# Optimization experiments

Hardware: AMD Instinct MI355X
Metric: run time of the kernel (lower is better)

The kernel has to match this reference:

```python
import jax, jax.numpy as jnp
import numpy as np
from jax import lax

TOP_K = 4
ROUTED_SCALING = 1.0
RENORMALIZE = True


def setup_inputs() -> dict:
    key = jax.random.key(0)
    ks = jax.random.split(key, 9)
    H, I, E = 2048, 1024, 16
    s = 0.02
    return {
        "hidden_states": jax.random.normal(ks[0], (2, 1024, H), jnp.float32),
        "gate_w": jax.random.normal(ks[1], (E, H), jnp.float32) * s,
        "expert_bias": jax.random.normal(ks[2], (E,), jnp.float32) * s,
        "w_gate": jax.random.normal(ks[3], (E, I, H), jnp.float32) * s,
        "w_up": jax.random.normal(ks[4], (E, I, H), jnp.float32) * s,
        "w_down": jax.random.normal(ks[5], (E, H, I), jnp.float32) * s,
        "sw_gate": jax.random.normal(ks[6], (I, H), jnp.float32) * s,
        "sw_up": jax.random.normal(ks[7], (I, H), jnp.float32) * s,
        "sw_down": jax.random.normal(ks[8], (H, I), jnp.float32) * s,
    }


def _swiglu_ffn(x, wg, wu, wd):
    # SiluAndMul(gate_up) -> down_proj
    return (jax.nn.silu(x @ wg.T) * (x @ wu.T)) @ wd.T


def reference(hidden_states, gate_w, expert_bias, w_gate, w_up, w_down,
              sw_gate, sw_up, sw_down):
    orig_shape = hidden_states.shape
    H = orig_shape[-1]
    x = hidden_states.reshape(-1, H)            # [T, H]
    T = x.shape[0]

    # --- sigmoid gating with score-correction bias (bias affects selection only) ---
    logits = x.astype(jnp.float32) @ gate_w.T    # [T, E] fp32 router
    scores = jax.nn.sigmoid(logits)
    _, topk_idx = lax.top_k(scores + expert_bias[None, :], TOP_K)   # [T, K]
    topk_w = jnp.take_along_axis(scores, topk_idx, axis=-1)         # raw scores
    if RENORMALIZE:
        topk_w = topk_w / jnp.sum(topk_w, axis=-1, keepdims=True)
    topk_w = topk_w * ROUTED_SCALING

    # scatter top-k weights into dense [T, E] combine matrix
    E = gate_w.shape[0]
    combine = jnp.zeros((T, E), dtype=x.dtype).at[
        jnp.arange(T)[:, None], topk_idx].set(topk_w.astype(x.dtype))

    # --- routed experts: scan over experts, weighted accumulate ---
    def step(acc, ws):
        wg, wu, wd, cw = ws                     # cw: [T] combine weights
        return acc + cw[:, None] * _swiglu_ffn(x, wg, wu, wd), None

    routed, _ = lax.scan(step, jnp.zeros_like(x),
                         (w_gate, w_up, w_down, combine.T))

    # --- shared expert ---
    shared = _swiglu_ffn(x, sw_gate, sw_up, sw_down)

    return (routed + shared).reshape(orig_shape)
```

## Files before the change

kernel.cpp:

```cpp
#include <hip/hip_runtime.h>
#include <hip/hip_bf16.h>
#include <cstdint>

#define TK 2048
#define HD 2048
#define ID 1024
#define NE 16
#define NG 17
#define TOPK 4
#define SLOTS (TK*TOPK)
#define ROWS_ALL (SLOTS+TK)
#define IH (ID*HD)
#define MAXT 96

typedef __attribute__((ext_vector_type(4))) float f32x4;
typedef __attribute__((ext_vector_type(16))) float f32x16;
typedef __attribute__((ext_vector_type(8))) short s16x8;
typedef unsigned short u16;
typedef unsigned long long u64;

__device__ __forceinline__ u16 f2bf(float f){
  union { float f; uint32_t u; } v; v.f = f;
  uint32_t r = v.u + 0x7fffu + ((v.u >> 16) & 1u);
  return (u16)(r >> 16);
}

#define GLD16(g, l) __builtin_amdgcn_global_load_lds( \
    (const __attribute__((address_space(1))) void*)(g), \
    (__attribute__((address_space(3))) void*)(l), 16, 0, 0)

__device__ __forceinline__ const s16x8* fragp(const u16* b, int row, int off){
  return (const s16x8*)((const char*)b + row*128 + (off ^ ((row&7)<<4)));
}
__device__ __forceinline__ int swz2(int r){
  return (r & 7) ^ (((r >> 3) & 3) << 1);
}
__device__ __forceinline__ const s16x8* fragp2(const u16* b, int row, int off){
  return (const s16x8*)((const char*)b + row*128 + (off ^ (swz2(row)<<4)));
}

#define MFMA16(a,b,c) __builtin_amdgcn_mfma_f32_16x16x32_bf16((a),(b),(c),0,0,0)
#define MFMA32(a,b,c) __builtin_amdgcn_mfma_f32_32x32x16_bf16((a),(b),(c),0,0,0)

__global__ void k_prep(const float* __restrict__ x, u16* __restrict__ xb,
                       u64* __restrict__ maskbits, int* __restrict__ tokcnt){
  int gi = blockIdx.x*blockDim.x + threadIdx.x;
  int st = gridDim.x*blockDim.x;
  if (gi < NE*32) maskbits[gi] = 0ull;
  if (gi < TK) tokcnt[gi] = 0;
  for (int i=gi; i<TK*HD/4; i+=st){
    float4 f = ((const float4*)x)[i];
    ushort4 o; o.x=f2bf(f.x); o.y=f2bf(f.y); o.z=f2bf(f.z); o.w=f2bf(f.w);
    ((ushort4*)xb)[i] = o;
  }
}

__global__ void k_cvtw(const float* __restrict__ wg, const float* __restrict__ wu,
                       const float* __restrict__ wd, const float* __restrict__ swg,
                       const float* __restrict__ swu, const float* __restrict__ swd,
                       u16* __restrict__ wgb, u16* __restrict__ wub, u16* __restrict__ wdb){
  const size_t nbig = (size_t)NE*IH/4, nsml = IH/4;
  const size_t total = 3*nbig + 3*nsml;
  for (size_t i = (size_t)blockIdx.x*blockDim.x + threadIdx.x; i < total;
       i += (size_t)gridDim.x*blockDim.x){
    const float4* src; ushort4* dst; size_t j = i;
    if (j < nbig){ src=(const float4*)wg + j;  dst=(ushort4*)wgb + j; }
    else if ((j-=nbig) < nbig){ src=(const float4*)wu + j;  dst=(ushort4*)wub + j; }
    else if ((j-=nbig) < nbig){ src=(const float4*)wd + j;  dst=(ushort4*)wdb + j; }
    else if ((j-=nbig) < nsml){ src=(const float4*)swg + j; dst=(ushort4*)wgb + nbig + j; }
    else if ((j-=nsml) < nsml){ src=(const float4*)swu + j; dst=(ushort4*)wub + nbig + j; }
    else { j-=nsml; src=(const float4*)swd + j; dst=(ushort4*)wdb + nbig + j; }
    float4 f = *src;
    ushort4 o; o.x=f2bf(f.x); o.y=f2bf(f.y); o.z=f2bf(f.z); o.w=f2bf(f.w);
    *dst = o;
  }
}

__global__ __launch_bounds__(256) void k_logits(const float* __restrict__ x,
                                                const float* __restrict__ gw,
                                                const float* __restrict__ bias,
                                                float* __restrict__ wdense,
                                                u64* __restrict__ maskbits){
  int t = blockIdx.x, tid = threadIdx.x;
  int lane = tid & 63, wv = tid >> 6;
  const float* xr = x + (size_t)t*HD;
  float acc[NE];
  #pragma unroll
  for (int e=0;e<NE;e++) acc[e]=0.f;
  for (int k=tid;k<HD;k+=256){
    float xv = xr[k];
    #pragma unroll
    for (int e=0;e<NE;e++) acc[e] += xv * gw[e*HD + k];
  }
  __shared__ float red[NE][4];
  #pragma unroll
  for (int e=0;e<NE;e++){
    float v = acc[e];
    #pragma unroll
    for (int off=32;off>0;off>>=1) v += __shfl_down(v, off, 64);
    if (lane==0) red[e][wv] = v;
  }
  __syncthreads();
  if (tid == 0){
    float sc[NE], bs[NE];
    #pragma unroll
    for (int e=0;e<NE;e++){
      float l = red[e][0]+red[e][1]+red[e][2]+red[e][3];
      float s = 1.f/(1.f+expf(-l));
      sc[e]=s; bs[e]=s+bias[e];
    }
    int idx[TOPK]; float wsum=0.f; unsigned used=0;
    for (int k=0;k<TOPK;k++){
      int best=0; float bv=-1e30f;
      for (int e=0;e<NE;e++) if (!((used>>e)&1u) && bs[e] > bv){ bv=bs[e]; best=e; }
      used |= 1u<<best; idx[k]=best; wsum += sc[best];
    }
    float inv = 1.f/wsum;
    for (int k=0;k<TOPK;k++){
      int e = idx[k];
      wdense[t*NE + e] = sc[e]*inv;
      atomicOr(&maskbits[e*32 + (t>>6)], 1ull << (t&63));
    }
  }
}

__global__ void k_scan(const u64* __restrict__ maskbits, int* __restrict__ counts,
                       int* __restrict__ offsets, int* __restrict__ wordpfx,
                       int* __restrict__ tiles){
  int acc = 0;
  for (int e=0;e<NE;e++){
    int c = 0;
    for (int w=0;w<32;w++){ wordpfx[e*32+w] = c; c += __popcll(maskbits[e*32+w]); }
    counts[e] = c;
  }
  for (int e=0;e<NE;e++){ offsets[e] = acc; acc += counts[e]; }
  offsets[NE] = acc;
  counts[NE] = TK;
  int nt = 0;
  for (int g=0; g<NG; g++){
    int c = counts[g];
    for (int mt=0; mt*128 < c && nt < MAXT; mt++) tiles[nt++] = (g<<8) | mt;
  }
  for (; nt<MAXT; nt++) tiles[nt] = -1;
}

__global__ void k_scatter(const u64* __restrict__ maskbits, const int* __restrict__ offsets,
                          const int* __restrict__ wordpfx, const float* __restrict__ wdense,
                          int* __restrict__ rowtok, float* __restrict__ roww,
                          int* __restrict__ tokcnt, int* __restrict__ tok4){
  int t = blockIdx.x*blockDim.x + threadIdx.x;
  int e = blockIdx.y;
  if (t >= TK) return;
  if (e == NE){ rowtok[offsets[NE]+t] = t; roww[offsets[NE]+t] = 1.f; return; }
  u64 w = maskbits[e*32 + (t>>6)];
  if ((w >> (t&63)) & 1ull){
    int pos = offsets[e] + wordpfx[e*32 + (t>>6)] + __popcll(w & ((1ull << (t&63)) - 1ull));
    rowtok[pos] = t; roww[pos] = wdense[t*NE + e];
    int r = atomicAdd(&tokcnt[t], 1);
    tok4[t*TOPK + r] = pos;
  }
}

__global__ __launch_bounds__(256) void k_gemm1b(
    const u16* __restrict__ xb, const u16* __restrict__ wgb, const u16* __restrict__ wub,
    const int* __restrict__ counts, const int* __restrict__ offsets,
    const int* __restrict__ rowtok, const float* __restrict__ roww,
    const int* __restrict__ tiles, u16* __restrict__ P)
{
  int te = tiles[blockIdx.y];
  if (te < 0) return;
  int g = te >> 8, mt = te & 255;
  int cnt = counts[g];
  int n0 = blockIdx.x*64;
  int base = offsets[g];
  const u16* wg16 = wgb + (size_t)g*IH;
  const u16* wu16 = wub + (size_t)g*IH;

  __shared__ u16 lsA[128*64];
  __shared__ u16 lsG[64*64];
  __shared__ u16 lsU[64*64];

  int tid = threadIdx.x, lane = tid & 63, wv = tid >> 6;
  int wm = (wv>>1)*64, wn = (wv&1)*32;
  int rl = lane & 15, hi = lane >> 4;

  f32x4 accg[4][2] = {}; f32x4 accu[4][2] = {};

  const u16* aSrc[4];
  #pragma unroll
  for (int i=0;i<4;i++){
    int b = i*256 + tid, r = b>>3, cb = b&7;
    int m = mt*128 + r; if (m >= cnt) m = cnt-1;
    int tok = rowtok[base + m];
    aSrc[i] = xb + (size_t)tok*HD + ((cb ^ (r&7))<<3);
  }
  const u16 *gSrc[2], *uSrc[2];
  #pragma unroll
  for (int i=0;i<2;i++){
    int b = i*256 + tid, r = b>>3, cb = b&7;
    size_t off = (size_t)(n0 + r)*HD + ((cb ^ (r&7))<<3);
    gSrc[i] = wg16 + off; uSrc[i] = wu16 + off;
  }

  for (int k0=0; k0<HD; k0+=64){
    #pragma unroll
    for (int i=0;i<4;i++) GLD16(aSrc[i]+k0, lsA + (i*256 + wv*64)*8);
    #pragma unroll
    for (int i=0;i<2;i++) GLD16(gSrc[i]+k0, lsG + (i*256 + wv*64)*8);
    #pragma unroll
    for (int i=0;i<2;i++) GLD16(uSrc[i]+k0, lsU + (i*256 + wv*64)*8);
    __syncthreads();
    #pragma unroll
    for (int ks=0; ks<2; ++ks){
      int off = ks*64 + hi*16;
      s16x8 af[4];
      #pragma unroll
      for (int mi=0;mi<4;mi++) af[mi] = *fragp(lsA, wm+16*mi+rl, off);
      #pragma unroll
      for (int ni=0;ni<2;ni++){
        s16x8 bg = *fragp(lsG, wn+16*ni+rl, off);
        s16x8 bu = *fragp(lsU, wn+16*ni+rl, off);
        #pragma unroll
        for (int mi=0;mi<4;mi++){
          accg[mi][ni] = MFMA16(af[mi], bg, accg[mi][ni]);
          accu[mi][ni] = MFMA16(af[mi], bu, accu[mi][ni]);
        }
      }
    }
    __syncthreads();
  }
  int rl4 = hi*4, cl = rl;
  #pragma unroll
  for (int mi=0;mi<4;mi++){
    #pragma unroll
    for (int j=0;j<4;j++){
      int m = mt*128 + wm + mi*16 + rl4 + j;
      if (m < cnt){
        int slot = base + m;
        float wgt = roww[slot];
        #pragma unroll
        for (int ni=0;ni<2;ni++){
          float gv = accg[mi][ni][j], uv = accu[mi][ni][j];
          float pv = gv/(1.f+expf(-gv))*uv*wgt;
          P[(size_t)slot*ID + n0 + wn + ni*16 + cl] = f2bf(pv);
        }
      }
    }
  }
}

__global__ __launch_bounds__(256, 2) void k_gemm2b(
    const u16* __restrict__ P, const u16* __restrict__ wdb,
    const int* __restrict__ counts, const int* __restrict__ offsets,
    const int* __restrict__ tiles, u16* __restrict__ R)
{
  int te = tiles[blockIdx.y];
  if (te < 0) return;
  int g = te >> 8, mt = te & 255;
  int cnt = counts[g];
  int base = offsets[g];
  int n0 = blockIdx.x*256;
  const u16* wd16 = wdb + (size_t)g*IH;

  __shared__ u16 lsA[128*64];
  __shared__ u16 lsB[256*64];

  int tid = threadIdx.x, lane = tid & 63, wv = tid >> 6;
  int wm = (wv>>1)*64, wn = (wv&1)*128;
  int rl = lane & 31, hi = lane >> 5;
  f32x16 acc[2][4] = {};

  const u16* aSrc[4];
  #pragma unroll
  for (int i=0;i<4;i++){
    int b = i*256 + tid, r = b>>3, cb = b&7;
    int m = mt*128 + r; if (m >= cnt) m = cnt-1;
    aSrc[i] = P + (size_t)(base + m)*ID + ((cb ^ swz2(r))<<3);
  }
  const u16* bSrc[8];
  #pragma unroll
  for (int i=0;i<8;i++){
    int b = i*256 + tid, r = b>>3, cb = b&7;
    bSrc[i] = wd16 + (size_t)(n0 + r)*ID + ((cb ^ swz2(r))<<3);
  }

  for (int t=0; t<ID/64; ++t){
    int k0 = t*64;
    #pragma unroll
    for (int i=0;i<4;i++) GLD16(aSrc[i]+k0, lsA + (i*256 + wv*64)*8);
    #pragma unroll
    for (int i=0;i<8;i++) GLD16(bSrc[i]+k0, lsB + (i*256 + wv*64)*8);
    asm volatile("s_waitcnt vmcnt(0)" ::: "memory");
    __builtin_amdgcn_s_barrier();
    #pragma unroll
    for (int s=0; s<4; ++s){
      int off = s*32 + hi*16;
      s16x8 af[2], bf[4];
      af[0] = *fragp2(lsA, wm + rl, off);
      af[1] = *fragp2(lsA, wm + 32 + rl, off);
      #pragma unroll
      for (int nj=0;nj<4;nj++) bf[nj] = *fragp2(lsB, wn + nj*32 + rl, off);
      #pragma unroll
      for (int mi=0;mi<2;mi++)
        #pragma unroll
        for (int nj=0;nj<4;nj++)
          acc[mi][nj] = MFMA32(af[mi], bf[nj], acc[mi][nj]);
    }
    asm volatile("s_waitcnt lgkmcnt(0)" ::: "memory");
    __builtin_amdgcn_s_barrier();
  }
  #pragma unroll
  for (int mi=0;mi<2;mi++){
    #pragma unroll
    for (int r=0;r<16;r++){
      int rowb = wm + mi*32 + (r&3) + 8*(r>>2) + 4*hi;
      int m = mt*128 + rowb;
      if (m < cnt){
        int slot = base + m;
        u16* rrow = R + (size_t)slot*HD + n0 + wn + rl;
        #pragma unroll
        for (int nj=0;nj<4;nj++) rrow[nj*32] = f2bf(acc[mi][nj][r]);
      }
    }
  }
}

__global__ __launch_bounds__(256) void k_reduce(const u16* __restrict__ R,
                                                const int* __restrict__ tok4,
                                                float* __restrict__ out){
  int t = blockIdx.x;
  int c0 = threadIdx.x * 8;
  int s0 = tok4[t*TOPK+0], s1 = tok4[t*TOPK+1], s2 = tok4[t*TOPK+2], s3 = tok4[t*TOPK+3];
  const ushort4* p0 = (const ushort4*)(R + (size_t)s0*HD + c0);
  const ushort4* p1 = (const ushort4*)(R + (size_t)s1*HD + c0);
  const ushort4* p2 = (const ushort4*)(R + (size_t)s2*HD + c0);
  const ushort4* p3 = (const ushort4*)(R + (size_t)s3*HD + c0);
  const ushort4* ps = (const ushort4*)(R + (size_t)(SLOTS + t)*HD + c0);
  float* o = out + (size_t)t*HD + c0;
  #pragma unroll
  for (int h=0; h<2; h++){
    ushort4 a = p0[h], b = p1[h], c = p2[h], d = p3[h], e = ps[h];
    #pragma unroll
    for (int j=0;j<4;j++){
      u16 ua = ((const u16*)&a)[j], ub = ((const u16*)&b)[j];
      u16 uc = ((const u16*)&c)[j], ud = ((const u16*)&d)[j], ue = ((const u16*)&e)[j];
      union { uint32_t u; float f; } w;
      float v;
      w.u = (uint32_t)ua<<16; v  = w.f;
      w.u = (uint32_t)ub<<16; v += w.f;
      w.u = (uint32_t)uc<<16; v += w.f;
      w.u = (uint32_t)ud<<16; v += w.f;
      w.u = (uint32_t)ue<<16; v += w.f;
      o[h*4 + j] = v;
    }
  }
}


extern "C" void kernel_launch(void* const* d_in, const int* in_sizes, int n_in,
                              void* d_out, int out_size, void* d_ws, size_t ws_size,
                              hipStream_t stream){
  (void)in_sizes; (void)n_in; (void)ws_size; (void)out_size;
  const float* x       = (const float*)d_in[0];
  const float* gate_w  = (const float*)d_in[1];
  const float* ebias   = (const float*)d_in[2];
  const float* w_gate  = (const float*)d_in[3];
  const float* w_up    = (const float*)d_in[4];
  const float* w_down  = (const float*)d_in[5];
  const float* sw_gate = (const float*)d_in[6];
  const float* sw_up   = (const float*)d_in[7];
  const float* sw_down = (const float*)d_in[8];
  float* out = (float*)d_out;

  char* p = (char*)d_ws;
  auto alloc = [&](size_t bytes)->char*{ char* r = p; p += (bytes + 255) & ~(size_t)255; return r; };
  u16*   xb       = (u16*)  alloc((size_t)TK*HD*2);
  u16*   P        = (u16*)  alloc((size_t)ROWS_ALL*ID*2);
  float* wdense   = (float*)alloc((size_t)TK*NE*4);
  u64*   maskbits = (u64*)  alloc((size_t)NE*32*8);
  int*   wordpfx  = (int*)  alloc((size_t)NE*32*4);
  int*   counts   = (int*)  alloc(64);
  int*   offsets  = (int*)  alloc(64);
  int*   tiles    = (int*)  alloc(MAXT*4);
  int*   rowtok   = (int*)  alloc((size_t)ROWS_ALL*4);
  float* roww     = (float*)alloc((size_t)ROWS_ALL*4);
  int*   tokcnt   = (int*)  alloc((size_t)TK*4);
  int*   tok4     = (int*)  alloc((size_t)TK*TOPK*4);
  size_t slab = (size_t)NG*IH*2;
  u16* wgb = (u16*)alloc(slab);
  u16* wub = (u16*)alloc(slab);
  u16* wdb = (u16*)alloc(slab);
  u16* R = wgb;

  k_prep<<<2048, 256, 0, stream>>>(x, xb, maskbits, tokcnt);
  k_cvtw<<<2048, 256, 0, stream>>>(w_gate, w_up, w_down, sw_gate, sw_up, sw_down,
                                   wgb, wub, wdb);
  k_logits<<<TK, 256, 0, stream>>>(x, gate_w, ebias, wdense, maskbits);
  k_scan<<<1, 1, 0, stream>>>(maskbits, counts, offsets, wordpfx, tiles);
  k_scatter<<<dim3(TK/256, NG), 256, 0, stream>>>(maskbits, offsets, wordpfx, wdense,
                                                  rowtok, roww, tokcnt, tok4);

  dim3 g1(ID/64, MAXT);
  k_gemm1b<<<g1, 256, 0, stream>>>(xb, wgb, wub, counts, offsets, rowtok, roww, tiles, P);
  dim3 g2(HD/256, MAXT);
  k_gemm2b<<<g2, 256, 0, stream>>>(P, wdb, counts, offsets, tiles, R);
  k_reduce<<<TK, 256, 0, stream>>>(R, tok4, out);
}
```

Measured before the change: 393.6 us.

## Fuse router logits with weight/activation conversion and swizzle GEMM tile order

Merges the activation bf16 conversion, the weight conversion and the router logits/top-k kernel into one launch: the first TK blocks do routing while the remaining blocks convert x and all weights. A small init kernel now zeroes the mask bits and counters. Both grouped GEMMs also remap their flat block index so that groups of 8 row tiles sweep the column tiles together, which should improve L2 reuse of weight tiles. This cuts launch count and lets routing overlap the memory-bound conversion, but the routing blocks may compete with the conversion blocks for bandwidth.

```diff
diff --git a/kernel.cpp b/kernel.cpp
--- a/kernel.cpp
+++ b/kernel.cpp
@@ -42,84 +42,82 @@
 #define MFMA16(a,b,c) __builtin_amdgcn_mfma_f32_16x16x32_bf16((a),(b),(c),0,0,0)
 #define MFMA32(a,b,c) __builtin_amdgcn_mfma_f32_32x32x16_bf16((a),(b),(c),0,0,0)
 
-__global__ void k_prep(const float* __restrict__ x, u16* __restrict__ xb,
-                       u64* __restrict__ maskbits, int* __restrict__ tokcnt){
+__global__ void k_init(u64* __restrict__ maskbits, int* __restrict__ tokcnt){
   int gi = blockIdx.x*blockDim.x + threadIdx.x;
-  int st = gridDim.x*blockDim.x;
   if (gi < NE*32) maskbits[gi] = 0ull;
   if (gi < TK) tokcnt[gi] = 0;
-  for (int i=gi; i<TK*HD/4; i+=st){
-    float4 f = ((const float4*)x)[i];
-    ushort4 o; o.x=f2bf(f.x); o.y=f2bf(f.y); o.z=f2bf(f.z); o.w=f2bf(f.w);
-    ((ushort4*)xb)[i] = o;
-  }
-}
-
-__global__ void k_cvtw(const float* __restrict__ wg, const float* __restrict__ wu,
-                       const float* __restrict__ wd, const float* __restrict__ swg,
-                       const float* __restrict__ swu, const float* __restrict__ swd,
-                       u16* __restrict__ wgb, u16* __restrict__ wub, u16* __restrict__ wdb){
-  const size_t nbig = (size_t)NE*IH/4, nsml = IH/4;
-  const size_t total = 3*nbig + 3*nsml;
-  for (size_t i = (size_t)blockIdx.x*blockDim.x + threadIdx.x; i < total;
-       i += (size_t)gridDim.x*blockDim.x){
-    const float4* src; ushort4* dst; size_t j = i;
-    if (j < nbig){ src=(const float4*)wg + j;  dst=(ushort4*)wgb + j; }
-    else if ((j-=nbig) < nbig){ src=(const float4*)wu + j;  dst=(ushort4*)wub + j; }
-    else if ((j-=nbig) < nbig){ src=(const float4*)wd + j;  dst=(ushort4*)wdb + j; }
-    else if ((j-=nbig) < nsml){ src=(const float4*)swg + j; dst=(ushort4*)wgb + nbig + j; }
-    else if ((j-=nsml) < nsml){ src=(const float4*)swu + j; dst=(ushort4*)wub + nbig + j; }
-    else { j-=nsml; src=(const float4*)swd + j; dst=(ushort4*)wdb + nbig + j; }
-    float4 f = *src;
-    ushort4 o; o.x=f2bf(f.x); o.y=f2bf(f.y); o.z=f2bf(f.z); o.w=f2bf(f.w);
-    *dst = o;
-  }
-}
-
-__global__ __launch_bounds__(256) void k_logits(const float* __restrict__ x,
-                                                const float* __restrict__ gw,
-                                                const float* __restrict__ bias,
-                                                float* __restrict__ wdense,
-                                                u64* __restrict__ maskbits){
-  int t = blockIdx.x, tid = threadIdx.x;
-  int lane = tid & 63, wv = tid >> 6;
-  const float* xr = x + (size_t)t*HD;
-  float acc[NE];
-  #pragma unroll
-  for (int e=0;e<NE;e++) acc[e]=0.f;
-  for (int k=tid;k<HD;k+=256){
-    float xv = xr[k];
-    #pragma unroll
-    for (int e=0;e<NE;e++) acc[e] += xv * gw[e*HD + k];
-  }
-  __shared__ float red[NE][4];
-  #pragma unroll
-  for (int e=0;e<NE;e++){
-    float v = acc[e];
-    #pragma unroll
-    for (int off=32;off>0;off>>=1) v += __shfl_down(v, off, 64);
-    if (lane==0) red[e][wv] = v;
-  }
-  __syncthreads();
-  if (tid == 0){
-    float sc[NE], bs[NE];
+}
+
+__global__ __launch_bounds__(256) void k_fused(
+    const float* __restrict__ x, const float* __restrict__ gw,
+    const float* __restrict__ bias,
+    const float* __restrict__ wg, const float* __restrict__ wu,
+    const float* __restrict__ wd, const float* __restrict__ swg,
+    const float* __restrict__ swu, const float* __restrict__ swd,
+    u16* __restrict__ xb, u16* __restrict__ wgb, u16* __restrict__ wub,
+    u16* __restrict__ wdb, float* __restrict__ wdense, u64* __restrict__ maskbits)
+{
+  int tid = threadIdx.x;
+  if (blockIdx.x < TK){
+    int t = blockIdx.x;
+    int lane = tid & 63, wv = tid >> 6;
+    const float* xr = x + (size_t)t*HD;
+    float acc[NE];
+    #pragma unroll
+    for (int e=0;e<NE;e++) acc[e]=0.f;
+    for (int k=tid;k<HD;k+=256){
+      float xv = xr[k];
+      #pragma unroll
+      for (int e=0;e<NE;e++) acc[e] += xv * gw[e*HD + k];
+    }
+    __shared__ float red[NE][4];
     #pragma unroll
     for (int e=0;e<NE;e++){
-      float l = red[e][0]+red[e][1]+red[e][2]+red[e][3];
-      float s = 1.f/(1.f+expf(-l));
-      sc[e]=s; bs[e]=s+bias[e];
-    }
-    int idx[TOPK]; float wsum=0.f; unsigned used=0;
-    for (int k=0;k<TOPK;k++){
-      int best=0; float bv=-1e30f;
-      for (int e=0;e<NE;e++) if (!((used>>e)&1u) && bs[e] > bv){ bv=bs[e]; best=e; }
-      used |= 1u<<best; idx[k]=best; wsum += sc[best];
-    }
-    float inv = 1.f/wsum;
-    for (int k=0;k<TOPK;k++){
-      int e = idx[k];
-      wdense[t*NE + e] = sc[e]*inv;
-      atomicOr(&maskbits[e*32 + (t>>6)], 1ull << (t&63));
+      float v = acc[e];
+      #pragma unroll
+      for (int off=32;off>0;off>>=1) v += __shfl_down(v, off, 64);
+      if (lane==0) red[e][wv] = v;
+    }
+    __syncthreads();
+    if (tid == 0){
+      float sc[NE], bs[NE];
+      #pragma unroll
+      for (int e=0;e<NE;e++){
+        float l = red[e][0]+red[e][1]+red[e][2]+red[e][3];
+        float s = 1.f/(1.f+expf(-l));
+        sc[e]=s; bs[e]=s+bias[e];
+      }
+      int idx[TOPK]; float wsum=0.f; unsigned used=0;
+      for (int k=0;k<TOPK;k++){
+        int best=0; float bv=-1e30f;
+        for (int e=0;e<NE;e++) if (!((used>>e)&1u) && bs[e] > bv){ bv=bs[e]; best=e; }
+        used |= 1u<<best; idx[k]=best; wsum += sc[best];
+      }
+      float inv = 1.f/wsum;
+      for (int k=0;k<TOPK;k++){
+        int e = idx[k];
+        wdense[t*NE + e] = sc[e]*inv;
+        atomicOr(&maskbits[e*32 + (t>>6)], 1ull << (t&63));
+      }
+    }
+  } else {
+    size_t bid = blockIdx.x - TK;
+    size_t nblk = gridDim.x - TK;
+    const size_t nx = (size_t)TK*HD/4;
+    const size_t nbig = (size_t)NE*IH/4, nsml = IH/4;
+    const size_t total = nx + 3*nbig + 3*nsml;
+    for (size_t i = bid*256 + tid; i < total; i += nblk*256){
+      const float4* src; ushort4* dst; size_t j = i;
+      if (j < nx){ src=(const float4*)x + j; dst=(ushort4*)xb + j; }
+      else if ((j-=nx) < nbig){ src=(const float4*)wg + j;  dst=(ushort4*)wgb + j; }
+      else if ((j-=nbig) < nbig){ src=(const float4*)wu + j;  dst=(ushort4*)wub + j; }
+      else if ((j-=nbig) < nbig){ src=(const float4*)wd + j;  dst=(ushort4*)wdb + j; }
+      else if ((j-=nbig) < nsml){ src=(const float4*)swg + j; dst=(ushort4*)wgb + nbig + j; }
+      else if ((j-=nsml) < nsml){ src=(const float4*)swu + j; dst=(ushort4*)wub + nbig + j; }
+      else { j-=nsml; src=(const float4*)swd + j; dst=(ushort4*)wdb + nbig + j; }
+      float4 f = *src;
+      ushort4 o; o.x=f2bf(f.x); o.y=f2bf(f.y); o.z=f2bf(f.z); o.w=f2bf(f.w);
+      *dst = o;
     }
   }
 }
@@ -167,11 +165,14 @@
     const int* __restrict__ rowtok, const float* __restrict__ roww,
     const int* __restrict__ tiles, u16* __restrict__ P)
 {
-  int te = tiles[blockIdx.y];
+  int flat = blockIdx.x + 16*blockIdx.y;
+  int tileIdx = (flat >> 7)*8 + (flat & 7);
+  int colIdx  = (flat & 127) >> 3;
+  int te = tiles[tileIdx];
   if (te < 0) return;
   int g = te >> 8, mt = te & 255;
   int cnt = counts[g];
-  int n0 = blockIdx.x*64;
+  int n0 = colIdx*64;
   int base = offsets[g];
   const u16* wg16 = wgb + (size_t)g*IH;
   const u16* wu16 = wub + (size_t)g*IH;
@@ -254,12 +255,15 @@
     const int* __restrict__ counts, const int* __restrict__ offsets,
     const int* __restrict__ tiles, u16* __restrict__ R)
 {
-  int te = tiles[blockIdx.y];
+  int flat = blockIdx.x + 8*blockIdx.y;
+  int tileIdx = (flat >> 6)*8 + (flat & 7);
+  int colIdx  = (flat & 63) >> 3;
+  int te = tiles[tileIdx];
   if (te < 0) return;
   int g = te >> 8, mt = te & 255;
   int cnt = counts[g];
   int base = offsets[g];
-  int n0 = blockIdx.x*256;
+  int n0 = colIdx*256;
   const u16* wd16 = wdb + (size_t)g*IH;
 
   __shared__ u16 lsA[128*64];
@@ -392,10 +396,10 @@
   u16* wdb = (u16*)alloc(slab);
   u16* R = wgb;
 
-  k_prep<<<2048, 256, 0, stream>>>(x, xb, maskbits, tokcnt);
-  k_cvtw<<<2048, 256, 0, stream>>>(w_gate, w_up, w_down, sw_gate, sw_up, sw_down,
-                                   wgb, wub, wdb);
-  k_logits<<<TK, 256, 0, stream>>>(x, gate_w, ebias, wdense, maskbits);
+  k_init<<<8, 256, 0, stream>>>(maskbits, tokcnt);
+  k_fused<<<TK + 2048, 256, 0, stream>>>(x, gate_w, ebias,
+                                         w_gate, w_up, w_down, sw_gate, sw_up, sw_down,
+                                         xb, wgb, wub, wdb, wdense, maskbits);
   k_scan<<<1, 1, 0, stream>>>(maskbits, counts, offsets, wordpfx, tiles);
   k_scatter<<<dim3(TK/256, NG), 256, 0, stream>>>(maskbits, offsets, wordpfx, wdense,
                                                   rowtok, roww, tokcnt, tok4);
```

Result: slower. 419.2 us (+6.5%).
